# Kernel tuning notes

Hardware: AMD Instinct MI355X
Metric: run time of the kernel (lower is better)

The kernel has to match this reference:

```python
import jax, jax.numpy as jnp
import numpy as np

NUM_POINTS = 17
T_MAX = 2.0
VAR_GAMMA = 1.0
EPS = 1e-8


def setup_inputs() -> dict:
    key = jax.random.key(0)
    k1, k2 = jax.random.split(key)
    embeddings = jax.random.normal(k1, (65536, 768), dtype=jnp.float32)
    directions = jax.random.normal(k2, (768, 64), dtype=jnp.float32)
    return {"embeddings": embeddings, "directions": directions}


def reference(embeddings, directions):
    z = embeddings.astype(jnp.float32)  # [B, D]

    # per-dim variance floor (torch .std is unbiased, ddof=1)
    cls_std = jnp.std(z, axis=0, ddof=1)
    var_floor = jnp.mean(jax.nn.relu(VAR_GAMMA - cls_std))

    # column-normalized random directions (F.normalize(dim=0))
    dirs = directions / jnp.linalg.norm(directions, axis=0, keepdims=True)
    proj = z @ dirs  # [B, S]
    std = jnp.std(proj, axis=0, ddof=1)
    proj = (proj - jnp.mean(proj, axis=0, keepdims=True)) / (std + EPS)

    # trapezoidal quadrature over t in (0, T_MAX]
    t = jnp.linspace(0.0, T_MAX, NUM_POINTS + 1)[1:]  # [T]
    dt = T_MAX / NUM_POINTS
    w = jnp.full((NUM_POINTS,), dt).at[0].set(dt / 2).at[-1].set(dt / 2)

    # ECF over all t at once: tp [T, B, S]
    tp = t[:, None, None] * proj[None]
    ecf_real = jnp.mean(jnp.cos(tp), axis=1)  # [T, S]
    ecf_imag = jnp.mean(jnp.sin(tp), axis=1)  # [T, S]
    ecf_sq = ecf_real ** 2 + ecf_imag ** 2
    tcf = jnp.exp(-0.5 * t ** 2)[:, None]  # [T, 1]
    per_t = jnp.mean(ecf_sq - 2.0 * ecf_real * tcf + tcf ** 2, axis=1)  # [T]
    total = jnp.sum(w * per_t)

    loss = total + var_floor
    return loss
```

## Files before the change

kernel.cpp:

```cpp
#include <hip/hip_runtime.h>
#include <math.h>

#define B_ROWS 65536
#define D_DIM  768
#define S_DIM  64
#define T_PTS  17

#define WS_COLSUM 0
#define WS_COLSQ  768
#define WS_PSUM   1536
#define WS_PSQ    1600
#define WS_ECFR   1664
#define WS_ECFI   2752
#define WS_BT_HI_S 7680
#define WS_PROJ   53248

typedef __attribute__((ext_vector_type(8))) short short8;
typedef __attribute__((ext_vector_type(4))) short short4v;
typedef __attribute__((ext_vector_type(4))) float float4v;

#define MFMA_BF16 __builtin_amdgcn_mfma_f32_16x16x32_bf16

static __device__ inline unsigned short f2bf(float x) {
    unsigned u = __float_as_uint(x);
    u += 0x7FFFu + ((u >> 16) & 1u);
    return (unsigned short)(u >> 16);
}
static __device__ inline float bf2f(unsigned short h) {
    return __uint_as_float(((unsigned)h) << 16);
}

__global__ void norm_kernel(const float* __restrict__ dirs, float* __restrict__ ws) {
    int s = blockIdx.x;
    int t = threadIdx.x;
    if (s < 60) ws[s * 64 + t] = 0.f;

    float sum = 0.f;
    #pragma unroll
    for (int j = 0; j < 12; ++j) {
        float v = dirs[(size_t)(t + j * 64) * S_DIM + s];
        sum += v * v;
    }
    #pragma unroll
    for (int m = 32; m; m >>= 1) sum += __shfl_xor(sum, m, 64);
    float invn = 1.0f / sqrtf(sum);

    unsigned short* bt_hi = (unsigned short*)ws + WS_BT_HI_S;
    #pragma unroll
    for (int j = 0; j < 12; ++j) {
        int k = t + j * 64;
        float v = dirs[(size_t)k * S_DIM + s] * invn;
        bt_hi[s * D_DIM + k] = f2bf(v);
    }
}

__global__ __launch_bounds__(256, 2) void main_kernel(const float* __restrict__ z,
                                                      float* __restrict__ ws) {
    __shared__ __align__(16) short zs_hi[128 * 72];
    __shared__ __align__(16) short zs_lo[128 * 72];
    __shared__ __align__(16) short bs[64 * 72];
    __shared__ float colacc[1536];
    __shared__ __align__(16) float cbuf[2 * 64 * 17];

    const unsigned short* bt_hi = (const unsigned short*)ws + WS_BT_HI_S;
    float* proj = ws + WS_PROJ;

    int tid = threadIdx.x;
    int tx = tid & 15, ty = tid >> 4;
    int l = tid & 63, l15 = l & 15, q = l >> 4;
    int waveId = tid >> 6;
    int waveRow = waveId * 32;
    size_t rowbase = (size_t)blockIdx.x * 128;

    #pragma unroll
    for (int j = 0; j < 6; ++j) colacc[tid + j * 256] = 0.f;

    float4 av[8];
    #pragma unroll
    for (int j = 0; j < 8; ++j)
        av[j] = *reinterpret_cast<const float4*>(
            z + (rowbase + ty + 16 * j) * D_DIM + tx * 4);

    float4v acc[2][4] = {};

    for (int c = 0; c < D_DIM / 64; ++c) {
        int kc = c * 64;

        int srow = tid >> 2;
        int kpart = (tid & 3) * 16;
        short8 b0 = *(const short8*)(bt_hi + (size_t)srow * D_DIM + kc + kpart);
        short8 b1 = *(const short8*)(bt_hi + (size_t)srow * D_DIM + kc + kpart + 8);

        float ps0 = 0, ps1 = 0, ps2 = 0, ps3 = 0;
        float pq0 = 0, pq1 = 0, pq2 = 0, pq3 = 0;
        #pragma unroll
        for (int j = 0; j < 8; ++j) {
            float4 v = av[j];
            int rr = ty + 16 * j;
            ps0 += v.x; pq0 = fmaf(v.x, v.x, pq0);
            ps1 += v.y; pq1 = fmaf(v.y, v.y, pq1);
            ps2 += v.z; pq2 = fmaf(v.z, v.z, pq2);
            ps3 += v.w; pq3 = fmaf(v.w, v.w, pq3);
            short4v h4, l4;
            h4.x = (short)f2bf(v.x); l4.x = (short)f2bf(v.x - bf2f((unsigned short)h4.x));
            h4.y = (short)f2bf(v.y); l4.y = (short)f2bf(v.y - bf2f((unsigned short)h4.y));
            h4.z = (short)f2bf(v.z); l4.z = (short)f2bf(v.z - bf2f((unsigned short)h4.z));
            h4.w = (short)f2bf(v.w); l4.w = (short)f2bf(v.w - bf2f((unsigned short)h4.w));
            *reinterpret_cast<short4v*>(&zs_hi[rr * 72 + tx * 4]) = h4;
            *reinterpret_cast<short4v*>(&zs_lo[rr * 72 + tx * 4]) = l4;
        }
        cbuf[(tx * 4 + 0) * 17 + ty] = ps0;  cbuf[1088 + (tx * 4 + 0) * 17 + ty] = pq0;
        cbuf[(tx * 4 + 1) * 17 + ty] = ps1;  cbuf[1088 + (tx * 4 + 1) * 17 + ty] = pq1;
        cbuf[(tx * 4 + 2) * 17 + ty] = ps2;  cbuf[1088 + (tx * 4 + 2) * 17 + ty] = pq2;
        cbuf[(tx * 4 + 3) * 17 + ty] = ps3;  cbuf[1088 + (tx * 4 + 3) * 17 + ty] = pq3;

        *(short8*)&bs[srow * 72 + kpart]     = b0;
        *(short8*)&bs[srow * 72 + kpart + 8] = b1;
        __syncthreads();

        int kn = (kc + 64 < D_DIM) ? kc + 64 : kc;
        #pragma unroll
        for (int j = 0; j < 8; ++j)
            av[j] = *reinterpret_cast<const float4*>(
                z + (rowbase + ty + 16 * j) * D_DIM + kn + tx * 4);

        if (tid < 128) {
            int which = tid >> 6, kcol = tid & 63;
            const float* src = cbuf + which * 1088 + kcol * 17;
            float v = 0.f;
            #pragma unroll
            for (int r = 0; r < 16; ++r) v += src[r];
            colacc[which * 768 + kc + kcol] += v;
        }

        short8 ah[2][2], al[2][2];
        #pragma unroll
        for (int rt = 0; rt < 2; ++rt) {
            int aoff = (waveRow + rt * 16 + l15) * 72 + q * 8;
            ah[rt][0] = *(const short8*)&zs_hi[aoff];
            ah[rt][1] = *(const short8*)&zs_hi[aoff + 32];
            al[rt][0] = *(const short8*)&zs_lo[aoff];
            al[rt][1] = *(const short8*)&zs_lo[aoff + 32];
        }
        #pragma unroll
        for (int st = 0; st < 4; ++st) {
            int boff = (st * 16 + l15) * 72 + q * 8;
            short8 bh0 = *(const short8*)&bs[boff];
            short8 bh1 = *(const short8*)&bs[boff + 32];
            #pragma unroll
            for (int rt = 0; rt < 2; ++rt) {
                acc[rt][st] = MFMA_BF16(ah[rt][0], bh0, acc[rt][st], 0, 0, 0);
                acc[rt][st] = MFMA_BF16(al[rt][0], bh0, acc[rt][st], 0, 0, 0);
                acc[rt][st] = MFMA_BF16(ah[rt][1], bh1, acc[rt][st], 0, 0, 0);
                acc[rt][st] = MFMA_BF16(al[rt][1], bh1, acc[rt][st], 0, 0, 0);
            }
        }
        __syncthreads();
    }

    #pragma unroll
    for (int j = 0; j < 6; ++j) {
        int idx = tid + j * 256;
        atomicAdd(&ws[idx], colacc[idx]);
    }

    #pragma unroll
    for (int rt = 0; rt < 2; ++rt)
        #pragma unroll
        for (int st = 0; st < 4; ++st) {
            int col = st * 16 + l15;
            size_t rbase = rowbase + waveRow + rt * 16 + q * 4;
            float4v v = acc[rt][st];
            proj[(rbase + 0) * S_DIM + col] = v[0];
            proj[(rbase + 1) * S_DIM + col] = v[1];
            proj[(rbase + 2) * S_DIM + col] = v[2];
            proj[(rbase + 3) * S_DIM + col] = v[3];
        }

    float* red = cbuf;
    #pragma unroll
    for (int st = 0; st < 4; ++st) {
        float cs = 0.f, cq = 0.f;
        #pragma unroll
        for (int rt = 0; rt < 2; ++rt) {
            float4v v = acc[rt][st];
            cs += v[0] + v[1] + v[2] + v[3];
            cq += v[0]*v[0] + v[1]*v[1] + v[2]*v[2] + v[3]*v[3];
        }
        int s = st * 16 + l15;
        int slot = waveId * 4 + q;
        red[(0 * 64 + s) * 16 + slot] = cs;
        red[(1 * 64 + s) * 16 + slot] = cq;
    }
    __syncthreads();
    if (tid < 128) {
        int which = tid >> 6, s = tid & 63;
        const float* src = red + (which * 64 + s) * 16;
        float v = 0.f;
        #pragma unroll
        for (int r = 0; r < 16; ++r) v += src[r];
        atomicAdd(&ws[(which ? WS_PSQ : WS_PSUM) + s], v);
    }
}

__global__ __launch_bounds__(256) void ecf_kernel(float* __restrict__ ws) {
    const float* proj = ws + WS_PROJ;
    int tid = threadIdx.x;
    int s = tid & 63, r = tid >> 6;

    __shared__ float s_mean[64], s_scale[64];
    if (tid < 64) {
        float sum = ws[WS_PSUM + tid], sq = ws[WS_PSQ + tid];
        float mean = sum / (float)B_ROWS;
        float var = (sq - (float)B_ROWS * mean * mean) / (float)(B_ROWS - 1);
        var = fmaxf(var, 0.f);
        s_mean[tid]  = mean;
        s_scale[tid] = 1.0f / (sqrtf(var) + 1e-8f);
    }
    __syncthreads();
    float mean  = s_mean[s];
    float scale = s_scale[s];
    const float dt = 2.0f / 17.0f;

    float ar[T_PTS] = {}, ai[T_PTS] = {};
    size_t base = (size_t)blockIdx.x * 64;
    for (int i = 0; i < 16; ++i) {
        size_t row = base + i * 4 + r;
        float p  = proj[row * S_DIM + s];
        float ph = (p - mean) * scale;
        float a  = dt * ph;
        float s1, c1;
        __sincosf(a, &s1, &c1);
        float cc = c1, sn = s1;
        ar[0] += cc; ai[0] += sn;
        #pragma unroll
        for (int k = 1; k < T_PTS; ++k) {
            float cn = cc * c1 - sn * s1;
            sn = fmaf(sn, c1, cc * s1);
            cc = cn;
            ar[k] += cc; ai[k] += sn;
        }
    }

    __shared__ float red[3 * 2 * T_PTS * 64];
    if (r > 0) {
        float* dst = red + (r - 1) * (2 * T_PTS * 64);
        #pragma unroll
        for (int k = 0; k < T_PTS; ++k) {
            dst[k * 64 + s]               = ar[k];
            dst[T_PTS * 64 + k * 64 + s]  = ai[k];
        }
    }
    __syncthreads();
    if (r == 0) {
        const int STRIDE = 2 * T_PTS * 64;
        #pragma unroll
        for (int k = 0; k < T_PTS; ++k) {
            float vr = ar[k] + red[k * 64 + s] + red[STRIDE + k * 64 + s]
                             + red[2 * STRIDE + k * 64 + s];
            float vi = ai[k] + red[T_PTS * 64 + k * 64 + s]
                             + red[STRIDE + T_PTS * 64 + k * 64 + s]
                             + red[2 * STRIDE + T_PTS * 64 + k * 64 + s];
            atomicAdd(&ws[WS_ECFR + k * 64 + s], vr);
            atomicAdd(&ws[WS_ECFI + k * 64 + s], vi);
        }
    }
}

__global__ __launch_bounds__(256) void loss_kernel(const float* __restrict__ ws,
                                                   float* __restrict__ out) {
    int tid = threadIdx.x;
    double local = 0.0;
    for (int d = tid; d < D_DIM; d += 256) {
        double sum = (double)ws[WS_COLSUM + d];
        double sq  = (double)ws[WS_COLSQ + d];
        double mean = sum / 65536.0;
        double var  = (sq - 65536.0 * mean * mean) / 65535.0;
        if (var < 0) var = 0;
        double rl = 1.0 - sqrt(var);
        if (rl < 0) rl = 0;
        local += rl / 768.0;
    }
    const double dt = 2.0 / 17.0;
    for (int idx = tid; idx < T_PTS * 64; idx += 256) {
        int i = idx >> 6;
        double t   = dt * (i + 1);
        double tcf = exp(-0.5 * t * t);
        double w   = (i == 0 || i == T_PTS - 1) ? dt * 0.5 : dt;
        double er = (double)ws[WS_ECFR + idx] / 65536.0;
        double ei = (double)ws[WS_ECFI + idx] / 65536.0;
        double term = er * er + ei * ei - 2.0 * er * tcf + tcf * tcf;
        local += w * term / 64.0;
    }
    __shared__ double red[256];
    red[tid] = local;
    __syncthreads();
    for (int off = 128; off > 0; off >>= 1) {
        if (tid < off) red[tid] += red[tid + off];
        __syncthreads();
    }
    if (tid == 0) out[0] = (float)red[0];
}

extern "C" void kernel_launch(void* const* d_in, const int* in_sizes, int n_in,
                              void* d_out, int out_size, void* d_ws, size_t ws_size,
                              hipStream_t stream) {
    const float* z    = (const float*)d_in[0];
    const float* dirs = (const float*)d_in[1];
    float* out = (float*)d_out;
    float* ws  = (float*)d_ws;

    norm_kernel<<<S_DIM, 64, 0, stream>>>(dirs, ws);
    main_kernel<<<B_ROWS / 128, 256, 0, stream>>>(z, ws);
    ecf_kernel<<<B_ROWS / 64, 256, 0, stream>>>(ws);
    loss_kernel<<<1, 256, 0, stream>>>(ws, out);
}
```

Before: 331.6 us.

## Drop bf16 lo-residual MFMA pass and simplify column-stat reductions in projection kernel

The projection GEMM now uses only a single bf16 rounding of z instead of the hi+lo split. This halves the MFMA count and removes the zs_lo LDS buffer. Column sum and sum-of-squares reductions now use wave shuffles plus LDS atomics instead of a padded cbuf transpose. The register prefetch of the next z chunk is removed, and launch bounds are raised to 3 blocks per CU to recover latency hiding through occupancy. Projection precision drops to plain bf16 inputs, which may loosen agreement with the fp32 reference after normalisation and the cos/sin terms.

```diff
diff --git a/kernel.cpp b/kernel.cpp
--- a/kernel.cpp
+++ b/kernel.cpp
@@ -26,9 +26,6 @@
     u += 0x7FFFu + ((u >> 16) & 1u);
     return (unsigned short)(u >> 16);
 }
-static __device__ inline float bf2f(unsigned short h) {
-    return __uint_as_float(((unsigned)h) << 16);
-}
 
 __global__ void norm_kernel(const float* __restrict__ dirs, float* __restrict__ ws) {
     int s = blockIdx.x;
@@ -45,24 +42,21 @@
     for (int m = 32; m; m >>= 1) sum += __shfl_xor(sum, m, 64);
     float invn = 1.0f / sqrtf(sum);
 
-    unsigned short* bt_hi = (unsigned short*)ws + WS_BT_HI_S;
+    unsigned short* bt = (unsigned short*)ws + WS_BT_HI_S;
     #pragma unroll
     for (int j = 0; j < 12; ++j) {
         int k = t + j * 64;
-        float v = dirs[(size_t)k * S_DIM + s] * invn;
-        bt_hi[s * D_DIM + k] = f2bf(v);
-    }
-}
-
-__global__ __launch_bounds__(256, 2) void main_kernel(const float* __restrict__ z,
+        bt[s * D_DIM + k] = f2bf(dirs[(size_t)k * S_DIM + s] * invn);
+    }
+}
+
+__global__ __launch_bounds__(256, 3) void main_kernel(const float* __restrict__ z,
                                                       float* __restrict__ ws) {
-    __shared__ __align__(16) short zs_hi[128 * 72];
-    __shared__ __align__(16) short zs_lo[128 * 72];
+    __shared__ __align__(16) short zs[128 * 72];
     __shared__ __align__(16) short bs[64 * 72];
     __shared__ float colacc[1536];
-    __shared__ __align__(16) float cbuf[2 * 64 * 17];
-
-    const unsigned short* bt_hi = (const unsigned short*)ws + WS_BT_HI_S;
+
+    const unsigned short* bt = (const unsigned short*)ws + WS_BT_HI_S;
     float* proj = ws + WS_PROJ;
 
     int tid = threadIdx.x;
@@ -74,73 +68,65 @@
 
     #pragma unroll
     for (int j = 0; j < 6; ++j) colacc[tid + j * 256] = 0.f;
-
-    float4 av[8];
-    #pragma unroll
-    for (int j = 0; j < 8; ++j)
-        av[j] = *reinterpret_cast<const float4*>(
-            z + (rowbase + ty + 16 * j) * D_DIM + tx * 4);
+    __syncthreads();
 
     float4v acc[2][4] = {};
 
     for (int c = 0; c < D_DIM / 64; ++c) {
         int kc = c * 64;
 
-        int srow = tid >> 2;
-        int kpart = (tid & 3) * 16;
-        short8 b0 = *(const short8*)(bt_hi + (size_t)srow * D_DIM + kc + kpart);
-        short8 b1 = *(const short8*)(bt_hi + (size_t)srow * D_DIM + kc + kpart + 8);
-
         float ps0 = 0, ps1 = 0, ps2 = 0, ps3 = 0;
         float pq0 = 0, pq1 = 0, pq2 = 0, pq3 = 0;
         #pragma unroll
         for (int j = 0; j < 8; ++j) {
-            float4 v = av[j];
             int rr = ty + 16 * j;
+            float4 v = *reinterpret_cast<const float4*>(
+                z + (rowbase + rr) * D_DIM + kc + tx * 4);
             ps0 += v.x; pq0 = fmaf(v.x, v.x, pq0);
             ps1 += v.y; pq1 = fmaf(v.y, v.y, pq1);
             ps2 += v.z; pq2 = fmaf(v.z, v.z, pq2);
             ps3 += v.w; pq3 = fmaf(v.w, v.w, pq3);
-            short4v h4, l4;
-            h4.x = (short)f2bf(v.x); l4.x = (short)f2bf(v.x - bf2f((unsigned short)h4.x));
-            h4.y = (short)f2bf(v.y); l4.y = (short)f2bf(v.y - bf2f((unsigned short)h4.y));
-            h4.z = (short)f2bf(v.z); l4.z = (short)f2bf(v.z - bf2f((unsigned short)h4.z));
-            h4.w = (short)f2bf(v.w); l4.w = (short)f2bf(v.w - bf2f((unsigned short)h4.w));
-            *reinterpret_cast<short4v*>(&zs_hi[rr * 72 + tx * 4]) = h4;
-            *reinterpret_cast<short4v*>(&zs_lo[rr * 72 + tx * 4]) = l4;
-        }
-        cbuf[(tx * 4 + 0) * 17 + ty] = ps0;  cbuf[1088 + (tx * 4 + 0) * 17 + ty] = pq0;
-        cbuf[(tx * 4 + 1) * 17 + ty] = ps1;  cbuf[1088 + (tx * 4 + 1) * 17 + ty] = pq1;
-        cbuf[(tx * 4 + 2) * 17 + ty] = ps2;  cbuf[1088 + (tx * 4 + 2) * 17 + ty] = pq2;
-        cbuf[(tx * 4 + 3) * 17 + ty] = ps3;  cbuf[1088 + (tx * 4 + 3) * 17 + ty] = pq3;
-
-        *(short8*)&bs[srow * 72 + kpart]     = b0;
-        *(short8*)&bs[srow * 72 + kpart + 8] = b1;
+            short4v h4;
+            h4.x = (short)f2bf(v.x); h4.y = (short)f2bf(v.y);
+            h4.z = (short)f2bf(v.z); h4.w = (short)f2bf(v.w);
+            *reinterpret_cast<short4v*>(&zs[rr * 72 + tx * 4]) = h4;
+        }
+
+        {
+            int srow = tid >> 2;
+            int kpart = (tid & 3) * 16;
+            short8 b0 = *(const short8*)(bt + (size_t)srow * D_DIM + kc + kpart);
+            short8 b1 = *(const short8*)(bt + (size_t)srow * D_DIM + kc + kpart + 8);
+            *(short8*)&bs[srow * 72 + kpart]     = b0;
+            *(short8*)&bs[srow * 72 + kpart + 8] = b1;
+        }
+
+        ps0 += __shfl_xor(ps0, 16, 64); ps0 += __shfl_xor(ps0, 32, 64);
+        ps1 += __shfl_xor(ps1, 16, 64); ps1 += __shfl_xor(ps1, 32, 64);
+        ps2 += __shfl_xor(ps2, 16, 64); ps2 += __shfl_xor(ps2, 32, 64);
+        ps3 += __shfl_xor(ps3, 16, 64); ps3 += __shfl_xor(ps3, 32, 64);
+        pq0 += __shfl_xor(pq0, 16, 64); pq0 += __shfl_xor(pq0, 32, 64);
+        pq1 += __shfl_xor(pq1, 16, 64); pq1 += __shfl_xor(pq1, 32, 64);
+        pq2 += __shfl_xor(pq2, 16, 64); pq2 += __shfl_xor(pq2, 32, 64);
+        pq3 += __shfl_xor(pq3, 16, 64); pq3 += __shfl_xor(pq3, 32, 64);
+        if (l < 16) {
+            atomicAdd(&colacc[kc + tx * 4 + 0], ps0);
+            atomicAdd(&colacc[kc + tx * 4 + 1], ps1);
+            atomicAdd(&colacc[kc + tx * 4 + 2], ps2);
+            atomicAdd(&colacc[kc + tx * 4 + 3], ps3);
+            atomicAdd(&colacc[768 + kc + tx * 4 + 0], pq0);
+            atomicAdd(&colacc[768 + kc + tx * 4 + 1], pq1);
+            atomicAdd(&colacc[768 + kc + tx * 4 + 2], pq2);
+            atomicAdd(&colacc[768 + kc + tx * 4 + 3], pq3);
+        }
         __syncthreads();
 
-        int kn = (kc + 64 < D_DIM) ? kc + 64 : kc;
-        #pragma unroll
-        for (int j = 0; j < 8; ++j)
-            av[j] = *reinterpret_cast<const float4*>(
-                z + (rowbase + ty + 16 * j) * D_DIM + kn + tx * 4);
-
-        if (tid < 128) {
-            int which = tid >> 6, kcol = tid & 63;
-            const float* src = cbuf + which * 1088 + kcol * 17;
-            float v = 0.f;
-            #pragma unroll
-            for (int r = 0; r < 16; ++r) v += src[r];
-            colacc[which * 768 + kc + kcol] += v;
-        }
-
-        short8 ah[2][2], al[2][2];
+        short8 ah[2][2];
         #pragma unroll
         for (int rt = 0; rt < 2; ++rt) {
             int aoff = (waveRow + rt * 16 + l15) * 72 + q * 8;
-            ah[rt][0] = *(const short8*)&zs_hi[aoff];
-            ah[rt][1] = *(const short8*)&zs_hi[aoff + 32];
-            al[rt][0] = *(const short8*)&zs_lo[aoff];
-            al[rt][1] = *(const short8*)&zs_lo[aoff + 32];
+            ah[rt][0] = *(const short8*)&zs[aoff];
+            ah[rt][1] = *(const short8*)&zs[aoff + 32];
         }
         #pragma unroll
         for (int st = 0; st < 4; ++st) {
@@ -150,9 +136,7 @@
             #pragma unroll
             for (int rt = 0; rt < 2; ++rt) {
                 acc[rt][st] = MFMA_BF16(ah[rt][0], bh0, acc[rt][st], 0, 0, 0);
-                acc[rt][st] = MFMA_BF16(al[rt][0], bh0, acc[rt][st], 0, 0, 0);
                 acc[rt][st] = MFMA_BF16(ah[rt][1], bh1, acc[rt][st], 0, 0, 0);
-                acc[rt][st] = MFMA_BF16(al[rt][1], bh1, acc[rt][st], 0, 0, 0);
             }
         }
         __syncthreads();
@@ -177,29 +161,36 @@
             proj[(rbase + 3) * S_DIM + col] = v[3];
         }
 
-    float* red = cbuf;
+    float* scratch = reinterpret_cast<float*>(zs);
+    float cs[4], cq[4];
     #pragma unroll
     for (int st = 0; st < 4; ++st) {
-        float cs = 0.f, cq = 0.f;
+        float s_ = 0.f, q_ = 0.f;
         #pragma unroll
         for (int rt = 0; rt < 2; ++rt) {
             float4v v = acc[rt][st];
-            cs += v[0] + v[1] + v[2] + v[3];
-            cq += v[0]*v[0] + v[1]*v[1] + v[2]*v[2] + v[3]*v[3];
-        }
-        int s = st * 16 + l15;
-        int slot = waveId * 4 + q;
-        red[(0 * 64 + s) * 16 + slot] = cs;
-        red[(1 * 64 + s) * 16 + slot] = cq;
+            s_ += v[0] + v[1] + v[2] + v[3];
+            q_ += v[0]*v[0] + v[1]*v[1] + v[2]*v[2] + v[3]*v[3];
+        }
+        s_ += __shfl_xor(s_, 16, 64); s_ += __shfl_xor(s_, 32, 64);
+        q_ += __shfl_xor(q_, 16, 64); q_ += __shfl_xor(q_, 32, 64);
+        cs[st] = s_; cq[st] = q_;
+    }
+    if (l < 16) {
+        #pragma unroll
+        for (int st = 0; st < 4; ++st) {
+            int col = st * 16 + l15;
+            scratch[(waveId * 64 + col) * 2 + 0] = cs[st];
+            scratch[(waveId * 64 + col) * 2 + 1] = cq[st];
+        }
     }
     __syncthreads();
     if (tid < 128) {
-        int which = tid >> 6, s = tid & 63;
-        const float* src = red + (which * 64 + s) * 16;
+        int which = tid >> 6, col = tid & 63;
         float v = 0.f;
         #pragma unroll
-        for (int r = 0; r < 16; ++r) v += src[r];
-        atomicAdd(&ws[(which ? WS_PSQ : WS_PSUM) + s], v);
+        for (int w = 0; w < 4; ++w) v += scratch[(w * 64 + col) * 2 + which];
+        atomicAdd(&ws[(which ? WS_PSQ : WS_PSUM) + col], v);
     }
 }
 
```

New measurement: 332.9 us. Within noise of the previous version (+0.4%).
